# Performance work log

Hardware: AMD Instinct MI355X
Metric: run time of the kernel (lower is better)

Reference implementation:

```python
import jax, jax.numpy as jnp
import numpy as np

# Architecture constants (from init_kwargs / ActionConfig)
R = 4          # vae_time_compression_ratio
WS = 2         # windows_size
PAD_T = R * WS # preprocessor left-padding
HID = 512      # action hidden_size
KD_IN = 16     # keyboard_dim_in (movement feature dim)
C_IMG = 3072   # img_hidden_size
KH = 1024      # keyboard_hidden_dim
NH = 16        # heads_num
HD = 64        # keyboard_head_dim
EPS = 1e-6


def setup_inputs() -> dict:
    key = jax.random.key(0)
    ks = jax.random.split(key, 8)
    B, T, Hs, Ws, NF = 1, 3, 44, 80, 81
    S = Hs * Ws

    def w(k, shape, s=0.02):
        return jax.random.normal(k, shape, jnp.float32) * s

    return {
        "x": jax.random.normal(ks[0], (B, T * S, C_IMG), jnp.float32),
        "condition": jax.random.normal(ks[1], (B, NF, KD_IN), jnp.float32),
        "me_w1": w(ks[2], (KD_IN, HID)), "me_b1": jnp.zeros((HID,), jnp.float32),
        "me_w2": w(ks[3], (HID, HID)), "me_b2": jnp.zeros((HID,), jnp.float32),
        "q_w": w(ks[4], (C_IMG, KH)), "q_b": jnp.zeros((KH,), jnp.float32),
        "kv_w": w(ks[5], (HID * WS * R, 2 * KH)), "kv_b": jnp.zeros((2 * KH,), jnp.float32),
        "qn_w": jnp.ones((HD,), jnp.float32), "kn_w": jnp.ones((HD,), jnp.float32),
        "out_w": w(ks[6], (KH, C_IMG)), "out_b": jnp.zeros((C_IMG,), jnp.float32),
        "H": Hs, "W": Ws, "T": T, "num_frame_per_block": T,
    }


def _rmsnorm(x, w):
    return x * jax.lax.rsqrt(jnp.mean(x * x, axis=-1, keepdims=True) + EPS) * w


def _preprocess(condition, me_w1, me_b1, me_w2, me_b2, num_frame_per_block):
    # MovementPreprocessor.forward with is_causal=True
    B, NF, _ = condition.shape
    pad = jnp.broadcast_to(condition[:, :1, :], (B, PAD_T, condition.shape[-1]))
    cp = jnp.concatenate([pad, condition], axis=1)            # [B, PAD_T+NF, KD_IN]
    emb = jax.nn.silu(cp @ me_w1 + me_b1) @ me_w2 + me_b2     # [B, PAD_T+NF, HID]
    n_feats = (NF - 1) // R + 1
    start = R * (n_feats - num_frame_per_block - WS) + PAD_T  # python int (static)
    emb = emb[:, start:, :]
    # vectorized replacement of the python-loop window slicing+stack
    win = jnp.arange(num_frame_per_block)[:, None] * R + jnp.arange(WS * R)[None, :]
    gm = emb[:, win, :]                                       # [B, L, WS*R, HID]
    return gm.reshape(B, num_frame_per_block, WS * R * HID)   # [B, L, 4096]


def reference(x, condition, me_w1, me_b1, me_w2, me_b2, q_w, q_b, kv_w, kv_b,
              qn_w, kn_w, out_w, out_b, H, W, T, num_frame_per_block):
    B = x.shape[0]
    S = H * W
    L = num_frame_per_block

    mf = _preprocess(condition, me_w1, me_b1, me_w2, me_b2, L)  # [B, L, HID*WS*R]

    # q: [B, T*S, C_IMG] -> [B, S, T, h, d]
    q = (x @ q_w + q_b).reshape(B, T, S, NH, HD).transpose(0, 2, 1, 3, 4)

    # k, v: [B, L, h, d] (NOT expanded over S; broadcast inside attention instead)
    kv = (mf @ kv_w + kv_b).reshape(B, L, 2, NH, HD)
    k, v = kv[:, :, 0], kv[:, :, 1]

    q = _rmsnorm(q, qn_w)
    k = _rmsnorm(k, kn_w)

    scale = 1.0 / np.sqrt(HD).astype(np.float32)
    scores = jnp.einsum('bsthd,blhd->bshtl', q, k) * scale      # [B,S,h,T,L]
    attn = jax.nn.softmax(scores, axis=-1)
    o = jnp.einsum('bshtl,blhd->bsthd', attn, v)                # [B,S,T,h,d]

    # '(B S) T H D -> B (T S) (H D)'
    o = o.transpose(0, 2, 1, 3, 4).reshape(B, T * S, NH * HD)
    return x + (o @ out_w + out_b)
```

## Files before the change

### kernel.cpp

```cpp
#include <hip/hip_runtime.h>

#define TOK  10560
#define CIMG 3072
#define KHD  1024

typedef unsigned short ushort_t;
typedef unsigned int u32;
using bf16x8 = __attribute__((ext_vector_type(8))) __bf16;
using f32x4  = __attribute__((ext_vector_type(4))) float;

#define GLD_LDS16(gp, lp) __builtin_amdgcn_global_load_lds( \
    (const __attribute__((address_space(1))) u32*)(gp), \
    (__attribute__((address_space(3))) u32*)(lp), 16, 0, 0)

static __device__ __forceinline__ unsigned short f2bf(float f){
  union { float f; unsigned u; } x; x.f = f;
  unsigned r = x.u + 0x7fffu + ((x.u >> 16) & 1u);
  return (unsigned short)(r >> 16);
}
static __device__ __forceinline__ float wave_sum(float v){
  #pragma unroll
  for (int off = 32; off > 0; off >>= 1) v += __shfl_xor(v, off, 64);
  return v;
}

__global__ __launch_bounds__(256) void k_pre1(const float* __restrict__ cond,
    const float* __restrict__ w1, const float* __restrict__ b1,
    float* __restrict__ h1){
  __shared__ float cs[16][16];
  int t = threadIdx.x;
  if (t < 256) cs[t >> 4][t & 15] = cond[(64 + (t >> 4)) * 16 + (t & 15)];
  __syncthreads();
  #pragma unroll
  for (int i = 0; i < 4; ++i){
    int idx = blockIdx.x * 256 + t + i * 2048;
    int r = idx >> 9, c = idx & 511;
    float s = b1[c];
    #pragma unroll
    for (int j = 0; j < 16; ++j) s += cs[r][j] * w1[j * 512 + c];
    h1[idx] = s / (1.f + __expf(-s));
  }
}

__global__ __launch_bounds__(256) void k_pre2(const float* __restrict__ h1,
    const float* __restrict__ w2, const float* __restrict__ b2,
    float* __restrict__ emb){
  int idx = blockIdx.x * 256 + threadIdx.x;
  int r = idx >> 9, c = idx & 511;
  const float* hp = h1 + r * 512;
  const float* wp = w2 + c;
  float acc = b2[c];
  #pragma unroll 8
  for (int j = 0; j < 512; ++j) acc += hp[j] * wp[(size_t)j * 512];
  emb[idx] = acc;
}

__global__ __launch_bounds__(256) void k_kv(const float* __restrict__ emb,
                                            const float* __restrict__ kvw,
                                            float* __restrict__ part){
  int bl = blockIdx.x;
  int l = bl / 128, rem = bl % 128, nt = rem / 16, kc = rem % 16;
  int n = nt * 256 + threadIdx.x;
  const float* e = emb + 2048 * l + kc * 256;
  const float* w = kvw + (size_t)(kc * 256) * 2048 + n;
  float acc = 0.f;
  for (int r = 0; r < 256; ++r) acc += e[r] * w[(size_t)r * 2048];
  part[kc * 6144 + l * 2048 + n] = acc;
}

__global__ void k_knorm(const float* __restrict__ part, const float* __restrict__ kvb,
                        const float* __restrict__ knw, float* __restrict__ kn,
                        float* __restrict__ vv){
  int wid = threadIdx.x >> 6, lane = threadIdx.x & 63;
  for (int i = 0; i < 12; ++i){
    int g = wid * 12 + i;
    int l = g >> 4, h = g & 15;
    int ik = l * 2048 + h * 64 + lane;
    float kk = kvb[h * 64 + lane];
    float v  = kvb[1024 + h * 64 + lane];
    for (int p = 0; p < 16; ++p){ kk += part[p * 6144 + ik]; v += part[p * 6144 + ik + 1024]; }
    float ss = wave_sum(kk * kk);
    kn[l * 1024 + h * 64 + lane] = kk * rsqrtf(ss * (1.f/64.f) + 1e-6f) * knw[lane];
    vv[l * 1024 + h * 64 + lane] = v;
  }
}

__global__ __launch_bounds__(256) void k_tconv(const float* __restrict__ src,
                                               ushort_t* __restrict__ dst,
                                               int R, int C){
  __shared__ float tile[32][33];
  int nTr = R >> 5;
  int tr = blockIdx.x % nTr, tc = blockIdx.x / nTr;
  int r0 = tr * 32, c0 = tc * 32, t = threadIdx.x;
  #pragma unroll
  for (int i = 0; i < 4; ++i){
    int idx = t + i * 256; int r = idx >> 5, c = idx & 31;
    tile[r][c] = src[(size_t)(r0 + r) * C + c0 + c];
  }
  __syncthreads();
  #pragma unroll
  for (int i = 0; i < 4; ++i){
    int idx = t + i * 256; int rr = idx >> 5, cc = idx & 31;
    dst[(size_t)(c0 + rr) * R + r0 + cc] = f2bf(tile[cc][rr]);
  }
}

__global__ __launch_bounds__(256) void k_xconv(const float* __restrict__ x,
                                               ushort_t* __restrict__ xb, int n4){
  for (int i = blockIdx.x * 256 + threadIdx.x; i < n4; i += gridDim.x * 256){
    float4 v = ((const float4*)x)[i];
    ushort4 o;
    o.x = f2bf(v.x); o.y = f2bf(v.y); o.z = f2bf(v.z); o.w = f2bf(v.w);
    ((ushort4*)xb)[i] = o;
  }
}

__global__ __launch_bounds__(512, 4) void gemm_fused(
    const ushort_t* __restrict__ A, const ushort_t* __restrict__ Bt,
    const float* __restrict__ bias, const float* __restrict__ kn,
    const float* __restrict__ qnw, float* __restrict__ acoef){
  __shared__ __align__(16) unsigned char lds[81920];
  const int tid = threadIdx.x;
  const int lane = tid & 63, wid = tid >> 6;
  const int wm = wid >> 1, wn = wid & 1;
  const int l15 = lane & 15, kg = lane >> 4;

  int bid = blockIdx.x;
  bid = (bid & 7) * 55 + (bid >> 3);
  const int mt = bid >> 3, nt = bid & 7;
  const int mbase = mt * 192, nbase = nt << 7;

  const int sr  = tid >> 1;
  const int skh = (tid & 1) ^ ((sr >> 2) & 1);
  const ushort_t* gA = A + (size_t)(mbase + sr) * CIMG + skh * 8;
  const int u   = tid - 384;
  const int skb = (u & 1) ^ ((u >> 3) & 1);
  const ushort_t* gB0 = Bt + (size_t)(nbase + (u >> 1)) * CIMG + skb * 8;
  const ushort_t* gB1 = gB0 + (size_t)64 * CIMG;

  auto stage = [&](int t, int c, int b){
    const int gk = t * 64 + c * 16;
    if (wid < 6){
      unsigned char* dst = lds + b * 40960 + c * 6144 + wid * 1024;
      GLD_LDS16(gA + gk, dst);
    } else {
      unsigned char* dst = lds + b * 40960 + 24576 + c * 4096 + (wid - 6) * 1024;
      GLD_LDS16(gB0 + gk, dst);
      GLD_LDS16(gB1 + gk, dst + 2048);
    }
  };
#define WAITC2 { if (wid < 6) asm volatile("s_waitcnt vmcnt(2)" ::: "memory"); \
                 else         asm volatile("s_waitcnt vmcnt(4)" ::: "memory"); }

  const int arl = wm * 48 + l15;
  const int brl = wn * 64 + l15;
  const int kh  = ((kg & 1) ^ ((l15 >> 2) & 1)) * 16;
  const unsigned aBase = (unsigned)((kg >> 1) * 6144 + arl * 32 + kh);
  const unsigned bBase = (unsigned)(24576 + (kg >> 1) * 4096 + brl * 32 + kh);

  f32x4 acc[3][4];
  #pragma unroll
  for (int m = 0; m < 3; ++m)
    #pragma unroll
    for (int n = 0; n < 4; ++n) acc[m][n] = {0.f, 0.f, 0.f, 0.f};

  bf16x8 afr[3], bfr[4];

#define PH_READ(base, KSL) { _Pragma("unroll") \
    for (int n = 0; n < 4; ++n) \
      bfr[n] = *(const bf16x8*)((base) + bBase + (KSL)*8192 + n*512); \
    _Pragma("unroll") \
    for (int m = 0; m < 3; ++m) \
      afr[m] = *(const bf16x8*)((base) + aBase + (KSL)*12288 + m*512); }
#define PH_MFMA { __builtin_amdgcn_s_setprio(1); _Pragma("unroll") \
    for (int m = 0; m < 3; ++m){ _Pragma("unroll") \
      for (int n = 0; n < 4; ++n) \
        acc[m][n] = __builtin_amdgcn_mfma_f32_16x16x32_bf16(afr[m], bfr[n], acc[m][n], 0, 0, 0); } \
    __builtin_amdgcn_s_setprio(0); }

  const int T = CIMG / 64;

  stage(0, 0, 0); stage(0, 1, 0); stage(0, 2, 0); stage(0, 3, 0);
  WAITC2;
  __builtin_amdgcn_s_barrier();

  for (int t = 0; t < T - 1; ++t){
    const int b = t & 1;
    const unsigned char* base = lds + b * 40960;
    PH_READ(base, 0);
    stage(t + 1, 0, b ^ 1); stage(t + 1, 1, b ^ 1);
    WAITC2;
    __builtin_amdgcn_s_barrier();
    PH_MFMA;
    __builtin_amdgcn_s_barrier();
    PH_READ(base, 1);
    stage(t + 1, 2, b ^ 1); stage(t + 1, 3, b ^ 1);
    WAITC2;
    __builtin_amdgcn_s_barrier();
    PH_MFMA;
    __builtin_amdgcn_s_barrier();
  }
  {
    const unsigned char* base = lds + ((T - 1) & 1) * 40960;
    PH_READ(base, 0);
    asm volatile("s_waitcnt vmcnt(0)" ::: "memory");
    __builtin_amdgcn_s_barrier();
    PH_MFMA;
    __builtin_amdgcn_s_barrier();
    PH_READ(base, 1);
    PH_MFMA;
  }
#undef PH_READ
#undef PH_MFMA
#undef WAITC2

  const int hglob = nt * 2 + wn;
  float qnwv[4], qbv[4], knv0[4], knv1[4], knv2[4];
  #pragma unroll
  for (int n = 0; n < 4; ++n){
    int d = n * 16 + l15;
    qnwv[n] = qnw[d];
    qbv[n]  = bias[nbase + wn * 64 + d];
    knv0[n] = kn[hglob * 64 + d];
    knv1[n] = kn[1024 + hglob * 64 + d];
    knv2[n] = kn[2048 + hglob * 64 + d];
  }
  #pragma unroll
  for (int m = 0; m < 3; ++m){
    #pragma unroll
    for (int j = 0; j < 4; ++j){
      float q[4], ssq = 0.f;
      #pragma unroll
      for (int n = 0; n < 4; ++n){ q[n] = acc[m][n][j] + qbv[n]; ssq += q[n] * q[n]; }
      #pragma unroll
      for (int off = 1; off < 16; off <<= 1) ssq += __shfl_xor(ssq, off, 64);
      float rs = rsqrtf(ssq * (1.f/64.f) + 1e-6f);
      float s0 = 0.f, s1 = 0.f, s2 = 0.f;
      #pragma unroll
      for (int n = 0; n < 4; ++n){
        float qn = q[n] * rs * qnwv[n];
        s0 += qn * knv0[n]; s1 += qn * knv1[n]; s2 += qn * knv2[n];
      }
      #pragma unroll
      for (int off = 1; off < 16; off <<= 1){
        s0 += __shfl_xor(s0, off, 64);
        s1 += __shfl_xor(s1, off, 64);
        s2 += __shfl_xor(s2, off, 64);
      }
      s0 *= 0.125f; s1 *= 0.125f; s2 *= 0.125f;
      float mx = fmaxf(s0, fmaxf(s1, s2));
      float e0 = __expf(s0 - mx), e1 = __expf(s1 - mx), e2 = __expf(s2 - mx);
      float inv = 1.f / (e0 + e1 + e2);
      int grow = mbase + wm * 48 + m * 16 + kg * 4 + j;
      if (l15 == 0){
        float2 a12 = {e1 * inv, e2 * inv};
        *(float2*)(acoef + (size_t)grow * 32 + hglob * 2) = a12;
      }
    }
  }
}

__global__ __launch_bounds__(512) void k_uv(const float* __restrict__ vv,
    const float* __restrict__ ow, float* __restrict__ U){
  int b = blockIdx.x;
  int i = b / 6, cc = b % 6;
  int h = i / 3, l = i % 3;
  int c = cc * 512 + threadIdx.x;
  const float* vp = vv + l * 1024 + h * 64;
  const float* wp = ow + (size_t)(h * 64) * 3072 + c;
  float acc = 0.f;
  #pragma unroll
  for (int d = 0; d < 64; ++d) acc += vp[d] * wp[(size_t)d * 3072];
  U[(size_t)i * 3072 + c] = acc;
}

__global__ __launch_bounds__(256) void k_ubase(const float* __restrict__ U,
    const float* __restrict__ ob, float* __restrict__ base, float* __restrict__ D){
  int c = blockIdx.x * 256 + threadIdx.x;
  float b = ob[c];
  #pragma unroll
  for (int h = 0; h < 16; ++h){
    float u0 = U[(size_t)(h * 3 + 0) * 3072 + c];
    float u1 = U[(size_t)(h * 3 + 1) * 3072 + c];
    float u2 = U[(size_t)(h * 3 + 2) * 3072 + c];
    b += u0;
    D[(size_t)(h * 2 + 0) * 3072 + c] = u1 - u0;
    D[(size_t)(h * 2 + 1) * 3072 + c] = u2 - u0;
  }
  base[c] = b;
}

__global__ __launch_bounds__(256) void k_rank32v(const float* __restrict__ x,
    const float* __restrict__ acoef, const float* __restrict__ D,
    const float* __restrict__ base, float* __restrict__ out){
  __shared__ __align__(16) float as[8][32];
  const int tid = threadIdx.x;
  const int rb = blockIdx.x / 3, cc = blockIdx.x % 3;
  const int r0 = rb * 8;
  const int c  = cc * 1024 + tid * 4;

  f32x4 xv[8];
  #pragma unroll
  for (int r = 0; r < 8; ++r)
    xv[r] = *(const f32x4*)(x + (size_t)(r0 + r) * 3072 + c);

  if (tid < 256) ((float*)as)[tid] = acoef[(size_t)r0 * 32 + tid];
  __syncthreads();

  f32x4 accv[8];
  #pragma unroll
  for (int r = 0; r < 8; ++r) accv[r] = {0.f, 0.f, 0.f, 0.f};

  #pragma unroll
  for (int k4 = 0; k4 < 8; ++k4){
    f32x4 d0 = *(const f32x4*)(D + (size_t)(k4 * 4 + 0) * 3072 + c);
    f32x4 d1 = *(const f32x4*)(D + (size_t)(k4 * 4 + 1) * 3072 + c);
    f32x4 d2 = *(const f32x4*)(D + (size_t)(k4 * 4 + 2) * 3072 + c);
    f32x4 d3 = *(const f32x4*)(D + (size_t)(k4 * 4 + 3) * 3072 + c);
    #pragma unroll
    for (int r = 0; r < 8; ++r){
      f32x4 a4 = *(const f32x4*)(&as[r][k4 * 4]);
      accv[r][0] += a4[0]*d0[0] + a4[1]*d1[0] + a4[2]*d2[0] + a4[3]*d3[0];
      accv[r][1] += a4[0]*d0[1] + a4[1]*d1[1] + a4[2]*d2[1] + a4[3]*d3[1];
      accv[r][2] += a4[0]*d0[2] + a4[1]*d1[2] + a4[2]*d2[2] + a4[3]*d3[2];
      accv[r][3] += a4[0]*d0[3] + a4[1]*d1[3] + a4[2]*d2[3] + a4[3]*d3[3];
    }
  }

  f32x4 b4 = *(const f32x4*)(base + c);
  #pragma unroll
  for (int r = 0; r < 8; ++r){
    const size_t o = (size_t)(r0 + r) * 3072 + c;
    f32x4 ov;
    ov[0] = xv[r][0] + b4[0] + accv[r][0];
    ov[1] = xv[r][1] + b4[1] + accv[r][1];
    ov[2] = xv[r][2] + b4[2] + accv[r][2];
    ov[3] = xv[r][3] + b4[3] + accv[r][3];
    *(f32x4*)(out + o) = ov;
  }
}

extern "C" void kernel_launch(void* const* d_in, const int* in_sizes, int n_in,
                              void* d_out, int out_size, void* d_ws, size_t ws_size,
                              hipStream_t stream){
  const float* x    = (const float*)d_in[0];
  const float* cond = (const float*)d_in[1];
  const float* mew1 = (const float*)d_in[2];
  const float* meb1 = (const float*)d_in[3];
  const float* mew2 = (const float*)d_in[4];
  const float* meb2 = (const float*)d_in[5];
  const float* qw   = (const float*)d_in[6];
  const float* qb   = (const float*)d_in[7];
  const float* kvw  = (const float*)d_in[8];
  const float* kvb  = (const float*)d_in[9];
  const float* qnw  = (const float*)d_in[10];
  const float* knw  = (const float*)d_in[11];
  const float* ow   = (const float*)d_in[12];
  const float* ob   = (const float*)d_in[13];

  char* ws = (char*)d_ws;
  float*    emb    = (float*)(ws + 0);
  float*    kvpart = (float*)(ws + 32768);
  float*    kn     = (float*)(ws + 425984);
  float*    vv     = (float*)(ws + 438272);
  ushort_t* qwt    = (ushort_t*)(ws + 450560);
  float*    U      = (float*)(ws + 6742016);
  float*    base   = (float*)(ws + 7331840);
  float*    Dbuf   = (float*)(ws + 7344128);
  float*    acoef  = (float*)(ws + 7737344);
  float*    h1buf  = (float*)(ws + 9089024);

  ushort_t* xb = (ushort_t*)d_out;

  k_pre1<<<8, 256, 0, stream>>>(cond, mew1, meb1, h1buf);
  k_pre2<<<32, 256, 0, stream>>>(h1buf, mew2, meb2, emb);
  k_kv<<<384, 256, 0, stream>>>(emb, kvw, kvpart);
  k_knorm<<<1, 256, 0, stream>>>(kvpart, kvb, knw, kn, vv);
  k_uv<<<288, 512, 0, stream>>>(vv, ow, U);
  k_ubase<<<12, 256, 0, stream>>>(U, ob, base, Dbuf);
  k_tconv<<<3072, 256, 0, stream>>>(qw, qwt, 3072, 1024);
  k_xconv<<<2048, 256, 0, stream>>>(x, xb, (TOK * CIMG) / 4);
  gemm_fused<<<440, 512, 0, stream>>>(xb, qwt, qb, kn, qnw, acoef);
  k_rank32v<<<3960, 256, 0, stream>>>(x, acoef, Dbuf, base, (float*)d_out);
}
```

Before: 281.5 us.

## Restructure Q-GEMM main loop to stage a full K-tile with one barrier per iteration

The double-buffered Q projection GEMM now issues all four K-chunks of the next tile at once and waits with vmcnt(0) plus a single barrier per 64-wide K step. Previously each step was split into two half-tiles with partial waits and four barriers. The aim is to cut barrier and synchronization overhead and let the MFMA work overlap a larger prefetch. The cost is that each iteration waits for the whole next tile to land, with less fine-grained overlap. The k_uv and k_ubase kernels are only moved within the file.

```diff
diff --git a/kernel.cpp b/kernel.cpp
--- a/kernel.cpp
+++ b/kernel.cpp
@@ -85,6 +85,36 @@
   }
 }
 
+__global__ __launch_bounds__(512) void k_uv(const float* __restrict__ vv,
+    const float* __restrict__ ow, float* __restrict__ U){
+  int b = blockIdx.x;
+  int i = b / 6, cc = b % 6;
+  int h = i / 3, l = i % 3;
+  int c = cc * 512 + threadIdx.x;
+  const float* vp = vv + l * 1024 + h * 64;
+  const float* wp = ow + (size_t)(h * 64) * 3072 + c;
+  float acc = 0.f;
+  #pragma unroll
+  for (int d = 0; d < 64; ++d) acc += vp[d] * wp[(size_t)d * 3072];
+  U[(size_t)i * 3072 + c] = acc;
+}
+
+__global__ __launch_bounds__(256) void k_ubase(const float* __restrict__ U,
+    const float* __restrict__ ob, float* __restrict__ base, float* __restrict__ D){
+  int c = blockIdx.x * 256 + threadIdx.x;
+  float b = ob[c];
+  #pragma unroll
+  for (int h = 0; h < 16; ++h){
+    float u0 = U[(size_t)(h * 3 + 0) * 3072 + c];
+    float u1 = U[(size_t)(h * 3 + 1) * 3072 + c];
+    float u2 = U[(size_t)(h * 3 + 2) * 3072 + c];
+    b += u0;
+    D[(size_t)(h * 2 + 0) * 3072 + c] = u1 - u0;
+    D[(size_t)(h * 2 + 1) * 3072 + c] = u2 - u0;
+  }
+  base[c] = b;
+}
+
 __global__ __launch_bounds__(256) void k_tconv(const float* __restrict__ src,
                                                ushort_t* __restrict__ dst,
                                                int R, int C){
@@ -138,19 +168,21 @@
   const ushort_t* gB0 = Bt + (size_t)(nbase + (u >> 1)) * CIMG + skb * 8;
   const ushort_t* gB1 = gB0 + (size_t)64 * CIMG;
 
-  auto stage = [&](int t, int c, int b){
-    const int gk = t * 64 + c * 16;
+  auto stage = [&](int t, int b){
+    const int gk = t * 64;
     if (wid < 6){
-      unsigned char* dst = lds + b * 40960 + c * 6144 + wid * 1024;
-      GLD_LDS16(gA + gk, dst);
+      #pragma unroll
+      for (int c = 0; c < 4; ++c)
+        GLD_LDS16(gA + gk + c * 16, lds + b * 40960 + c * 6144 + wid * 1024);
     } else {
-      unsigned char* dst = lds + b * 40960 + 24576 + c * 4096 + (wid - 6) * 1024;
-      GLD_LDS16(gB0 + gk, dst);
-      GLD_LDS16(gB1 + gk, dst + 2048);
+      #pragma unroll
+      for (int c = 0; c < 4; ++c){
+        unsigned char* dst = lds + b * 40960 + 24576 + c * 4096 + (wid - 6) * 1024;
+        GLD_LDS16(gB0 + gk + c * 16, dst);
+        GLD_LDS16(gB1 + gk + c * 16, dst + 2048);
+      }
     }
   };
-#define WAITC2 { if (wid < 6) asm volatile("s_waitcnt vmcnt(2)" ::: "memory"); \
-                 else         asm volatile("s_waitcnt vmcnt(4)" ::: "memory"); }
 
   const int arl = wm * 48 + l15;
   const int brl = wn * 64 + l15;
@@ -180,39 +212,21 @@
 
   const int T = CIMG / 64;
 
-  stage(0, 0, 0); stage(0, 1, 0); stage(0, 2, 0); stage(0, 3, 0);
-  WAITC2;
-  __builtin_amdgcn_s_barrier();
-
-  for (int t = 0; t < T - 1; ++t){
-    const int b = t & 1;
-    const unsigned char* base = lds + b * 40960;
-    PH_READ(base, 0);
-    stage(t + 1, 0, b ^ 1); stage(t + 1, 1, b ^ 1);
-    WAITC2;
-    __builtin_amdgcn_s_barrier();
-    PH_MFMA;
-    __builtin_amdgcn_s_barrier();
-    PH_READ(base, 1);
-    stage(t + 1, 2, b ^ 1); stage(t + 1, 3, b ^ 1);
-    WAITC2;
-    __builtin_amdgcn_s_barrier();
-    PH_MFMA;
-    __builtin_amdgcn_s_barrier();
-  }
-  {
-    const unsigned char* base = lds + ((T - 1) & 1) * 40960;
-    PH_READ(base, 0);
+  stage(0, 0);
+
+  for (int t = 0; t < T; ++t){
+    const unsigned char* base = lds + (t & 1) * 40960;
     asm volatile("s_waitcnt vmcnt(0)" ::: "memory");
     __builtin_amdgcn_s_barrier();
+    asm volatile("" ::: "memory");
+    PH_READ(base, 0);
+    if (t + 1 < T) stage(t + 1, (t + 1) & 1);
     PH_MFMA;
-    __builtin_amdgcn_s_barrier();
     PH_READ(base, 1);
     PH_MFMA;
   }
 #undef PH_READ
 #undef PH_MFMA
-#undef WAITC2
 
   const int hglob = nt * 2 + wn;
   float qnwv[4], qbv[4], knv0[4], knv1[4], knv2[4];
@@ -258,36 +272,6 @@
       }
     }
   }
-}
-
-__global__ __launch_bounds__(512) void k_uv(const float* __restrict__ vv,
-    const float* __restrict__ ow, float* __restrict__ U){
-  int b = blockIdx.x;
-  int i = b / 6, cc = b % 6;
-  int h = i / 3, l = i % 3;
-  int c = cc * 512 + threadIdx.x;
-  const float* vp = vv + l * 1024 + h * 64;
-  const float* wp = ow + (size_t)(h * 64) * 3072 + c;
-  float acc = 0.f;
-  #pragma unroll
-  for (int d = 0; d < 64; ++d) acc += vp[d] * wp[(size_t)d * 3072];
-  U[(size_t)i * 3072 + c] = acc;
-}
-
-__global__ __launch_bounds__(256) void k_ubase(const float* __restrict__ U,
-    const float* __restrict__ ob, float* __restrict__ base, float* __restrict__ D){
-  int c = blockIdx.x * 256 + threadIdx.x;
-  float b = ob[c];
-  #pragma unroll
-  for (int h = 0; h < 16; ++h){
-    float u0 = U[(size_t)(h * 3 + 0) * 3072 + c];
-    float u1 = U[(size_t)(h * 3 + 1) * 3072 + c];
-    float u2 = U[(size_t)(h * 3 + 2) * 3072 + c];
-    b += u0;
-    D[(size_t)(h * 2 + 0) * 3072 + c] = u1 - u0;
-    D[(size_t)(h * 2 + 1) * 3072 + c] = u2 - u0;
-  }
-  base[c] = b;
 }
 
 __global__ __launch_bounds__(256) void k_rank32v(const float* __restrict__ x,
```

Result: faster. 271.0 us (-3.7%).
